# Performance work log

Hardware: AMD Instinct MI355X
Metric: run time of the kernel (lower is better)

Reference implementation:

```python
import jax, jax.numpy as jnp
import numpy as np

N_NODES = 100000
N_EDGES = 1600000
N_PAIRS = 200000
IN_C, HID_C, OUT_C = 128, 128, 64


def setup_inputs() -> dict:
    key = jax.random.key(0)
    ks = jax.random.split(key, 10)
    x = jax.random.normal(ks[0], (N_NODES, IN_C), dtype=jnp.float32)
    edge_index = jax.random.randint(ks[1], (2, N_EDGES), 0, N_NODES, dtype=jnp.int64)
    node_i = jax.random.randint(ks[2], (N_PAIRS,), 0, N_NODES, dtype=jnp.int64)
    node_j = jax.random.randint(ks[3], (N_PAIRS,), 0, N_NODES, dtype=jnp.int64)
    def glorot(k, fan_in, fan_out):
        s = jnp.sqrt(6.0 / (fan_in + fan_out))
        return jax.random.uniform(k, (fan_in, fan_out), jnp.float32, -s, s)
    W1 = glorot(ks[4], IN_C, HID_C)
    b1 = jnp.zeros((HID_C,), jnp.float32)
    W2 = glorot(ks[5], HID_C, HID_C)
    b2 = jnp.zeros((HID_C,), jnp.float32)
    W3 = glorot(ks[6], HID_C, OUT_C)
    b3 = jnp.zeros((OUT_C,), jnp.float32)
    return {"x": x, "edge_index": edge_index, "node_i": node_i, "node_j": node_j,
            "W1": W1, "b1": b1, "W2": W2, "b2": b2, "W3": W3, "b3": b3}


def _gcn_layer(h, src, dst, deg_inv, w_e, W, b):
    # h: [N, Cin] -> linear then symmetric-normalized aggregation (with self loops)
    h = h @ W  # [N, Cout]
    msg = h[src] * w_e[:, None]  # [E, Cout] gather + edge weight
    agg = jax.ops.segment_sum(msg, dst, num_segments=N_NODES)
    agg = agg + h * deg_inv[:, None]  # self-loop term: h_i / deg_i
    return agg + b


def reference(x, edge_index, node_i, node_j, W1, b1, W2, b2, W3, b3):
    src, dst = edge_index[0], edge_index[1]
    # GCN normalization with self loops: deg_i = 1 + in-degree
    ones = jnp.ones((N_EDGES,), jnp.float32)
    deg = jax.ops.segment_sum(ones, dst, num_segments=N_NODES) + 1.0
    dinv_sqrt = jax.lax.rsqrt(deg)
    deg_inv = 1.0 / deg
    w_e = dinv_sqrt[src] * dinv_sqrt[dst]  # [E]

    h = _gcn_layer(x, src, dst, deg_inv, w_e, W1, b1)
    h = jax.nn.relu(h)  # dropout is identity in eval mode
    h = _gcn_layer(h, src, dst, deg_inv, w_e, W2, b2)
    h = jax.nn.relu(h)
    h = _gcn_layer(h, src, dst, deg_inv, w_e, W3, b3)

    # dot-product link decode (decode_type=None)
    return jnp.sum(h[node_i] * h[node_j], axis=-1)  # [N_PAIRS]
```

## Files before the change

kernel.cpp:

```cpp
#include <hip/hip_runtime.h>

#define NN 100000
#define NNP 100032
#define NE 1600000
#define NP 200000
#define NBKT 782
#define BCAP 3072
#define BKB 4096

typedef short s16x8 __attribute__((ext_vector_type(8)));
typedef float f32x4 __attribute__((ext_vector_type(4)));
typedef float f32x2 __attribute__((ext_vector_type(2)));

__device__ __forceinline__ unsigned short f2bf(float f) {
  unsigned int u = __float_as_uint(f);
  u += 0x7fffu + ((u >> 16) & 1u);
  return (unsigned short)(u >> 16);
}

__device__ __forceinline__ void pkadd(f32x2& a, uint u) {
  f32x2 v;
  v.x = __uint_as_float(u << 16);
  v.y = __uint_as_float(u & 0xffff0000u);
  asm("v_pk_add_f32 %0, %0, %1" : "+v"(a) : "v"(v));
}

__device__ __forceinline__ void rowadd(uint4 v, f32x2* a) {
  pkadd(a[0], v.x);
  pkadd(a[1], v.y);
  pkadd(a[2], v.z);
  pkadd(a[3], v.w);
}

template <int RSH>
__device__ __forceinline__ void gath(const int* __restrict__ col,
                                     const char* __restrict__ Tb, int s,
                                     int tend, uint co, f32x2* acc) {
  const int d = tend - s;
  const int nfull = d >> 3;
  const int rem = d & 7;
  int e = s;
  int c[8];
#pragma unroll
  for (int j = 0; j < 8; ++j) c[j] = col[e + j];
#pragma unroll 1
  for (int it = 0; it < nfull; ++it) {
    uint4 v0 = *(const uint4*)(Tb + (((uint)c[0] << RSH) | co));
    uint4 v1 = *(const uint4*)(Tb + (((uint)c[1] << RSH) | co));
    uint4 v2 = *(const uint4*)(Tb + (((uint)c[2] << RSH) | co));
    uint4 v3 = *(const uint4*)(Tb + (((uint)c[3] << RSH) | co));
    uint4 v4 = *(const uint4*)(Tb + (((uint)c[4] << RSH) | co));
    uint4 v5 = *(const uint4*)(Tb + (((uint)c[5] << RSH) | co));
    uint4 v6 = *(const uint4*)(Tb + (((uint)c[6] << RSH) | co));
    uint4 v7 = *(const uint4*)(Tb + (((uint)c[7] << RSH) | co));
    e += 8;
#pragma unroll
    for (int j = 0; j < 8; ++j) c[j] = col[e + j];
    rowadd(v0, acc);
    rowadd(v1, acc);
    rowadd(v2, acc);
    rowadd(v3, acc);
    rowadd(v4, acc);
    rowadd(v5, acc);
    rowadd(v6, acc);
    rowadd(v7, acc);
  }
  if (rem) {
#pragma unroll
    for (int j = 0; j < 8; ++j) c[j] = (j < rem) ? c[j] : NN;
    uint4 v0 = *(const uint4*)(Tb + (((uint)c[0] << RSH) | co));
    uint4 v1 = *(const uint4*)(Tb + (((uint)c[1] << RSH) | co));
    uint4 v2 = *(const uint4*)(Tb + (((uint)c[2] << RSH) | co));
    uint4 v3 = *(const uint4*)(Tb + (((uint)c[3] << RSH) | co));
    uint4 v4 = *(const uint4*)(Tb + (((uint)c[4] << RSH) | co));
    uint4 v5 = *(const uint4*)(Tb + (((uint)c[5] << RSH) | co));
    uint4 v6 = *(const uint4*)(Tb + (((uint)c[6] << RSH) | co));
    uint4 v7 = *(const uint4*)(Tb + (((uint)c[7] << RSH) | co));
    rowadd(v0, acc);
    rowadd(v1, acc);
    rowadd(v2, acc);
    rowadd(v3, acc);
    rowadd(v4, acc);
    rowadd(v5, acc);
    rowadd(v6, acc);
    rowadd(v7, acc);
  }
}

template <int NT>
__device__ __forceinline__ void prepw_dev(const float* __restrict__ W,
                                          uint* __restrict__ Wt, int tid) {
  constexpr int COUT = NT * 16;
  if (tid >= 4 * NT * 64) return;
  int lane = tid & 63, comb = tid >> 6;
  int ks = comb / NT, tl = comb % NT;
  int q = lane >> 4, n = lane & 15;
  uint w[4];
#pragma unroll
  for (int jj = 0; jj < 4; ++jj) {
    int k0 = ks * 32 + q * 8 + 2 * jj;
    uint lo = f2bf(W[k0 * COUT + tl * 16 + n]);
    uint hi = f2bf(W[(k0 + 1) * COUT + tl * 16 + n]);
    w[jj] = lo | (hi << 16);
  }
  ((uint4*)Wt)[comb * 64 + lane] = make_uint4(w[0], w[1], w[2], w[3]);
}

__global__ __launch_bounds__(256) void k_setup(const float* __restrict__ W1,
                                               const float* __restrict__ W2,
                                               const float* __restrict__ W3,
                                               uint* __restrict__ Wt1,
                                               uint* __restrict__ Wt2,
                                               uint* __restrict__ Wt3,
                                               int* __restrict__ gcur) {
  int b = blockIdx.x, t = threadIdx.x;
  if (b < 4) {
    int i = b * 256 + t;
    if (i < 1024) gcur[i] = 0;
  } else if (b < 12) {
    prepw_dev<8>(W1, Wt1, (b - 4) * 256 + t);
  } else if (b < 20) {
    prepw_dev<8>(W2, Wt2, (b - 12) * 256 + t);
  } else {
    prepw_dev<4>(W3, Wt3, (b - 20) * 256 + t);
  }
}

__global__ __launch_bounds__(256) void k_bucket(const int* __restrict__ ei,
                                                int* __restrict__ gcur,
                                                int* __restrict__ aux) {
  __shared__ int cnt[1024];
  __shared__ int scn[1024];
  __shared__ int cur[1024];
  __shared__ int sc[256];
  __shared__ int sorted[BKB];
  __shared__ unsigned short sbkt[BKB];
  const int t = threadIdx.x;
  const int base = blockIdx.x * BKB;

  for (int i = t; i < 1024; i += 256) cnt[i] = 0;
  __syncthreads();

  int pk[16], bk[16];
#pragma unroll
  for (int i = 0; i < 16; ++i) {
    int e = base + t + 256 * i;
    if (e < NE) {
      int src = ei[e], dst = ei[NE + e];
      bk[i] = dst >> 7;
      pk[i] = src | ((dst & 127) << 17);
      atomicAdd(&cnt[bk[i]], 1);
    } else {
      bk[i] = -1;
    }
  }
  __syncthreads();

  int s0 = cnt[4 * t], s1 = cnt[4 * t + 1], s2 = cnt[4 * t + 2], s3 = cnt[4 * t + 3];
  int local = s0 + s1 + s2 + s3;
  sc[t] = local;
  __syncthreads();
  for (int off = 1; off < 256; off <<= 1) {
    int a = (t >= off) ? sc[t - off] : 0;
    __syncthreads();
    sc[t] += a;
    __syncthreads();
  }
  int b0 = sc[t] - local;
  scn[4 * t] = b0;
  scn[4 * t + 1] = b0 + s0;
  scn[4 * t + 2] = b0 + s0 + s1;
  scn[4 * t + 3] = b0 + s0 + s1 + s2;
  cur[4 * t] = scn[4 * t];
  cur[4 * t + 1] = scn[4 * t + 1];
  cur[4 * t + 2] = scn[4 * t + 2];
  cur[4 * t + 3] = scn[4 * t + 3];
  __syncthreads();
  const int tot = sc[255];

#pragma unroll
  for (int i = 0; i < 16; ++i) {
    if (bk[i] >= 0) {
      int pos = atomicAdd(&cur[bk[i]], 1);
      sorted[pos] = pk[i];
      sbkt[pos] = (unsigned short)bk[i];
    }
  }
  __syncthreads();

  for (int b = t; b < 1024; b += 256) {
    int c = cnt[b];
    if (c > 0) cur[b] = b * BCAP + atomicAdd(&gcur[b], c);
  }
  __syncthreads();

  for (int k = t; k < tot; k += 256) {
    int b = sbkt[k];
    aux[cur[b] + (k - scn[b])] = sorted[k];
  }
}

__global__ __launch_bounds__(256) void k_csr(const int* __restrict__ gcur,
                                             const int* __restrict__ aux,
                                             int* __restrict__ row_ptr,
                                             float* __restrict__ dinv,
                                             int* __restrict__ col) {
  __shared__ int red[256];
  __shared__ int c[128];
  __shared__ int cur[128];
  const int b = blockIdx.x, t = threadIdx.x;
  int p = 0;
  for (int i = t; i < b; i += 256) p += gcur[i];
  red[t] = p;
  if (t < 128) c[t] = 0;
  __syncthreads();
  for (int off = 128; off > 0; off >>= 1) {
    if (t < off) red[t] += red[t + off];
    __syncthreads();
  }
  const int base = red[0];
  const int m = gcur[b];
  const int* a = aux + (size_t)b * BCAP;
  __syncthreads();
  for (int k = t; k < m; k += 256) atomicAdd(&c[a[k] >> 17], 1);
  __syncthreads();
  int val = (t < 128) ? c[t] : 0;
  red[t] = val;
  __syncthreads();
  for (int off = 1; off < 128; off <<= 1) {
    int add = (t >= off && t < 128) ? red[t - off] : 0;
    __syncthreads();
    if (t < 128) red[t] += add;
    __syncthreads();
  }
  if (t < 128) {
    int excl = red[t] - val + base;
    int node = b * 128 + t;
    if (node < NN) {
      row_ptr[node] = excl;
      dinv[node] = rsqrtf((float)(val + 1));
      cur[t] = excl;
    }
  }
  if (b == NBKT - 1 && t == 0) row_ptr[NN] = base + m;
  __syncthreads();
  for (int k = t; k < m; k += 256) {
    int pk2 = a[k];
    int pos = atomicAdd(&cur[pk2 >> 17], 1);
    col[pos] = pk2 & 0x1FFFF;
  }
}

__global__ __launch_bounds__(256) void k_gemm1(const float* __restrict__ A,
                                               const uint* __restrict__ Wt,
                                               const float* __restrict__ dinv,
                                               unsigned short* __restrict__ T) {
  constexpr int NT = 8, COUT = 128;
  __shared__ __align__(16) uint Wlds[4 * NT * 64 * 4];
  __shared__ __align__(16) unsigned short Obuf[64 * COUT];
  const int t = threadIdx.x;
  {
    const uint4* src = (const uint4*)Wt;
    uint4* dst = (uint4*)Wlds;
    for (int i = t; i < 4 * NT * 64; i += 256) dst[i] = src[i];
  }
  __syncthreads();

  const int wv = t >> 6, lane = t & 63;
  const int n = lane & 15, quad = lane >> 4;
  const int rbase = blockIdx.x * 64 + wv * 16;

  union AB { uint4 u; s16x8 s; };
  AB a[4];
  {
    int row = rbase + n;
    if (row >= NN) row = NN - 1;
    const float* ap = A + (size_t)row * 128;
#pragma unroll
    for (int ks = 0; ks < 4; ++ks) {
      float4 v0 = *(const float4*)(ap + ks * 32 + quad * 8);
      float4 v1 = *(const float4*)(ap + ks * 32 + quad * 8 + 4);
      a[ks].u.x = (uint)f2bf(v0.x) | ((uint)f2bf(v0.y) << 16);
      a[ks].u.y = (uint)f2bf(v0.z) | ((uint)f2bf(v0.w) << 16);
      a[ks].u.z = (uint)f2bf(v1.x) | ((uint)f2bf(v1.y) << 16);
      a[ks].u.w = (uint)f2bf(v1.z) | ((uint)f2bf(v1.w) << 16);
    }
  }

  f32x4 acc[NT];
#pragma unroll
  for (int tl = 0; tl < NT; ++tl) acc[tl] = (f32x4){0.f, 0.f, 0.f, 0.f};

#pragma unroll
  for (int ks = 0; ks < 4; ++ks) {
#pragma unroll
    for (int tl = 0; tl < NT; ++tl) {
      AB b;
      b.u = *(const uint4*)&Wlds[((ks * NT + tl) * 64 + lane) * 4];
      acc[tl] = __builtin_amdgcn_mfma_f32_16x16x32_bf16(a[ks].s, b.s, acc[tl], 0, 0, 0);
    }
  }

  float4 dv = *(const float4*)(dinv + rbase + quad * 4);
  float dvv[4] = {dv.x, dv.y, dv.z, dv.w};
  unsigned short* ob = Obuf + wv * 16 * COUT;
#pragma unroll
  for (int tl = 0; tl < NT; ++tl)
#pragma unroll
    for (int r = 0; r < 4; ++r)
      ob[(quad * 4 + r) * COUT + tl * 16 + n] = f2bf(acc[tl][r] * dvv[r]);

  uint4* gdst = (uint4*)(T + (size_t)rbase * COUT);
#pragma unroll
  for (int i = 0; i < 4; ++i) {
    int off16 = i * 64 + lane;
    int lrow = (off16 * 8) / COUT;
    uint4 v = make_uint4(0u, 0u, 0u, 0u);
    if (rbase + lrow < NN) v = *(const uint4*)&ob[off16 * 8];
    gdst[off16] = v;
  }
}

template <int COUT>
__global__ __launch_bounds__(256) void k_gg(const int* __restrict__ row_ptr,
                                            const int* __restrict__ col,
                                            const uint4* __restrict__ T4,
                                            const float* __restrict__ dinv,
                                            const float* __restrict__ bias,
                                            const uint4* __restrict__ Wt,
                                            unsigned short* __restrict__ Tout) {
  constexpr int NT = COUT / 16;
  constexpr int TLW = NT / 4;
  constexpr int OSTR = COUT + 8;
  __shared__ __align__(16) uint4 Alds[16 * 17];
  const int t = threadIdx.x, wv = t >> 6, lane = t & 63;
  const int nbase = blockIdx.x * 16;
  const int q = lane >> 4, cl = lane & 15;

  const int node = nbase + wv * 4 + q;
  int s = 0, tend = 0;
  if (node < NN) {
    s = row_ptr[node];
    tend = row_ptr[node + 1];
  }
  const char* Tb = (const char*)T4;
  const uint co = (uint)cl << 4;
  f32x2 acc[4];
  acc[0] = (f32x2){0.f, 0.f};
  acc[1] = (f32x2){0.f, 0.f};
  acc[2] = (f32x2){0.f, 0.f};
  acc[3] = (f32x2){0.f, 0.f};
  rowadd(*(const uint4*)(Tb + (((uint)node << 8) | co)), acc);
  gath<8>(col, Tb, s, tend, co, acc);

  {
    float dv = dinv[node];
    float4 b0 = *(const float4*)&bias[cl * 8];
    float4 b1 = *(const float4*)&bias[cl * 8 + 4];
    float r0 = fmaxf(fmaf(dv, acc[0].x, b0.x), 0.f);
    float r1 = fmaxf(fmaf(dv, acc[0].y, b0.y), 0.f);
    float r2 = fmaxf(fmaf(dv, acc[1].x, b0.z), 0.f);
    float r3 = fmaxf(fmaf(dv, acc[1].y, b0.w), 0.f);
    float r4 = fmaxf(fmaf(dv, acc[2].x, b1.x), 0.f);
    float r5 = fmaxf(fmaf(dv, acc[2].y, b1.y), 0.f);
    float r6 = fmaxf(fmaf(dv, acc[3].x, b1.z), 0.f);
    float r7 = fmaxf(fmaf(dv, acc[3].y, b1.w), 0.f);
    uint4 o;
    o.x = (uint)f2bf(r0) | ((uint)f2bf(r1) << 16);
    o.y = (uint)f2bf(r2) | ((uint)f2bf(r3) << 16);
    o.z = (uint)f2bf(r4) | ((uint)f2bf(r5) << 16);
    o.w = (uint)f2bf(r6) | ((uint)f2bf(r7) << 16);
    Alds[(wv * 4 + q) * 17 + cl] = o;
  }
  __syncthreads();

  const int n = lane & 15, quad = lane >> 4;
  union AB { uint4 u; s16x8 s; };
  AB a[4];
#pragma unroll
  for (int ks = 0; ks < 4; ++ks) a[ks].u = Alds[n * 17 + ks * 4 + quad];
  f32x4 acc2[TLW];
#pragma unroll
  for (int j = 0; j < TLW; ++j) acc2[j] = (f32x4){0.f, 0.f, 0.f, 0.f};
#pragma unroll
  for (int ks = 0; ks < 4; ++ks) {
#pragma unroll
    for (int j = 0; j < TLW; ++j) {
      int tl = wv * TLW + j;
      AB b;
      b.u = Wt[(ks * NT + tl) * 64 + lane];
      acc2[j] = __builtin_amdgcn_mfma_f32_16x16x32_bf16(a[ks].s, b.s, acc2[j], 0, 0, 0);
    }
  }
  __syncthreads();

  unsigned short* Obuf = (unsigned short*)Alds;
  float4 dv4 = *(const float4*)(dinv + nbase + quad * 4);
  float dvv[4] = {dv4.x, dv4.y, dv4.z, dv4.w};
#pragma unroll
  for (int j = 0; j < TLW; ++j) {
    int tl = wv * TLW + j;
#pragma unroll
    for (int r = 0; r < 4; ++r)
      Obuf[(quad * 4 + r) * OSTR + tl * 16 + n] = f2bf(acc2[j][r] * dvv[r]);
  }
  __syncthreads();

  if constexpr (COUT == 128) {
    int row = t >> 4, c16 = t & 15;
    uint4 v = make_uint4(0u, 0u, 0u, 0u);
    if (nbase + row < NN) v = *(const uint4*)&Obuf[row * OSTR + c16 * 8];
    ((uint4*)(Tout + (size_t)nbase * COUT))[row * 16 + c16] = v;
  } else {
    if (t < 128) {
      int row = t >> 3, c16 = t & 7;
      uint4 v = make_uint4(0u, 0u, 0u, 0u);
      if (nbase + row < NN) v = *(const uint4*)&Obuf[row * OSTR + c16 * 8];
      ((uint4*)(Tout + (size_t)nbase * COUT))[row * 8 + c16] = v;
    }
  }
}

__global__ __launch_bounds__(256) void k_gather3(const int* __restrict__ row_ptr,
                                                 const int* __restrict__ col,
                                                 const uint4* __restrict__ T4,
                                                 uint4* __restrict__ G3) {
  const int wid = (blockIdx.x * 256 + threadIdx.x) >> 6;
  const int lane = threadIdx.x & 63;
  const int g = lane >> 3, cl = lane & 7;
  const int node = wid * 8 + g;
  if (node >= NN) return;
  int s = row_ptr[node], tend = row_ptr[node + 1];
  const char* Tb = (const char*)T4;
  const uint co = (uint)cl << 4;
  f32x2 acc[4];
  acc[0] = (f32x2){0.f, 0.f};
  acc[1] = (f32x2){0.f, 0.f};
  acc[2] = (f32x2){0.f, 0.f};
  acc[3] = (f32x2){0.f, 0.f};
  rowadd(*(const uint4*)(Tb + (((uint)node << 7) | co)), acc);
  gath<7>(col, Tb, s, tend, co, acc);
  uint4 o;
  o.x = (uint)f2bf(acc[0].x) | ((uint)f2bf(acc[0].y) << 16);
  o.y = (uint)f2bf(acc[1].x) | ((uint)f2bf(acc[1].y) << 16);
  o.z = (uint)f2bf(acc[2].x) | ((uint)f2bf(acc[2].y) << 16);
  o.w = (uint)f2bf(acc[3].x) | ((uint)f2bf(acc[3].y) << 16);
  G3[(size_t)node * 8 + cl] = o;
}

__global__ __launch_bounds__(256) void k_decode(const int* __restrict__ ni,
                                                const int* __restrict__ nj,
                                                const uint2* __restrict__ G3,
                                                const float* __restrict__ dinv,
                                                const float* __restrict__ b3,
                                                float* __restrict__ out) {
  int p = blockIdx.x * 16 + (threadIdx.x >> 4);
  int cl = threadIdx.x & 15;
  int i = ni[p], j = nj[p];
  uint2 ui = G3[(size_t)i * 16 + cl];
  uint2 uj = G3[(size_t)j * 16 + cl];
  float4 bb = *(const float4*)&b3[cl * 4];
  float di = dinv[i], dj = dinv[j];
  float gi0 = __uint_as_float(ui.x << 16), gi1 = __uint_as_float(ui.x & 0xffff0000u);
  float gi2 = __uint_as_float(ui.y << 16), gi3 = __uint_as_float(ui.y & 0xffff0000u);
  float gj0 = __uint_as_float(uj.x << 16), gj1 = __uint_as_float(uj.x & 0xffff0000u);
  float gj2 = __uint_as_float(uj.y << 16), gj3 = __uint_as_float(uj.y & 0xffff0000u);
  float v = fmaf(di, gi0, bb.x) * fmaf(dj, gj0, bb.x) +
            fmaf(di, gi1, bb.y) * fmaf(dj, gj1, bb.y) +
            fmaf(di, gi2, bb.z) * fmaf(dj, gj2, bb.z) +
            fmaf(di, gi3, bb.w) * fmaf(dj, gj3, bb.w);
  v += __shfl_xor(v, 1, 64);
  v += __shfl_xor(v, 2, 64);
  v += __shfl_xor(v, 4, 64);
  v += __shfl_xor(v, 8, 64);
  if (cl == 0) out[p] = v;
}

extern "C" void kernel_launch(void* const* d_in, const int* in_sizes, int n_in,
                              void* d_out, int out_size, void* d_ws, size_t ws_size,
                              hipStream_t stream) {
  const float* x  = (const float*)d_in[0];
  const int*   ei = (const int*)d_in[1];
  const int*   ni = (const int*)d_in[2];
  const int*   nj = (const int*)d_in[3];
  const float* W1 = (const float*)d_in[4];
  const float* b1 = (const float*)d_in[5];
  const float* W2 = (const float*)d_in[6];
  const float* b2 = (const float*)d_in[7];
  const float* W3 = (const float*)d_in[8];
  const float* b3 = (const float*)d_in[9];
  float* out = (float*)d_out;

  float* dinv    = (float*)d_ws;
  int*   row_ptr = (int*)(dinv + 102400);
  int*   gcur    = row_ptr + 102400;
  int*   col     = gcur + 1024;
  uint*  Wt1     = (uint*)(col + NE);
  uint*  Wt2     = Wt1 + 8192;
  uint*  Wt3     = Wt2 + 8192;
  uint*  Tbf     = Wt3 + 4096;
  uint*  T2      = Tbf + (size_t)NNP * 64;
  uint*  G3      = T2 + (size_t)NNP * 64;
  int*   aux     = (int*)G3;

  k_setup<<<24, 256, 0, stream>>>(W1, W2, W3, Wt1, Wt2, Wt3, gcur);
  k_bucket<<<(NE + BKB - 1) / BKB, 256, 0, stream>>>(ei, gcur, aux);
  k_csr<<<NBKT, 256, 0, stream>>>(gcur, aux, row_ptr, dinv, col);

  const int GB = NNP / 64;
  const int FB = NNP / 16;
  const int GATB = NN / 32;

  k_gemm1<<<GB, 256, 0, stream>>>(x, Wt1, dinv, (unsigned short*)Tbf);
  k_gg<128><<<FB, 256, 0, stream>>>(row_ptr, col, (const uint4*)Tbf, dinv, b1,
                                    (const uint4*)Wt2, (unsigned short*)T2);
  k_gg<64><<<FB, 256, 0, stream>>>(row_ptr, col, (const uint4*)T2, dinv, b2,
                                   (const uint4*)Wt3, (unsigned short*)Tbf);
  k_gather3<<<GATB, 256, 0, stream>>>(row_ptr, col, (const uint4*)Tbf, (uint4*)G3);
  k_decode<<<NP / 16, 256, 0, stream>>>(ni, nj, (const uint2*)G3, dinv, b3, out);
}
```

Baseline: 305.5 us.

## Process nodes in degree-sorted order in aggregation kernels for load balance

Builds a degree histogram during CSR construction, scans it, and computes a permutation that groups nodes by in-degree. The fused gather+GEMM kernels and the final gather kernel then process nodes in this permuted order, so wavefronts handle neighbors of similar length and lanes within a wave diverge less. Output rows are scattered back to original node positions. This adds two small kernels, extra indirection loads, and loses contiguous output stores and locality of self-row reads.

```diff
diff --git a/kernel.cpp b/kernel.cpp
--- a/kernel.cpp
+++ b/kernel.cpp
@@ -112,7 +112,8 @@
                                                uint* __restrict__ Wt1,
                                                uint* __restrict__ Wt2,
                                                uint* __restrict__ Wt3,
-                                               int* __restrict__ gcur) {
+                                               int* __restrict__ gcur,
+                                               int* __restrict__ dhist) {
   int b = blockIdx.x, t = threadIdx.x;
   if (b < 4) {
     int i = b * 256 + t;
@@ -121,8 +122,10 @@
     prepw_dev<8>(W1, Wt1, (b - 4) * 256 + t);
   } else if (b < 20) {
     prepw_dev<8>(W2, Wt2, (b - 12) * 256 + t);
+  } else if (b < 24) {
+    prepw_dev<4>(W3, Wt3, (b - 20) * 256 + t);
   } else {
-    prepw_dev<4>(W3, Wt3, (b - 20) * 256 + t);
+    for (int i = t; i < 2048; i += 256) dhist[i] = 0;
   }
 }
 
@@ -204,11 +207,14 @@
                                              const int* __restrict__ aux,
                                              int* __restrict__ row_ptr,
                                              float* __restrict__ dinv,
-                                             int* __restrict__ col) {
+                                             int* __restrict__ col,
+                                             int* __restrict__ dhist) {
   __shared__ int red[256];
   __shared__ int c[128];
   __shared__ int cur[128];
+  __shared__ int lh[1024];
   const int b = blockIdx.x, t = threadIdx.x;
+  for (int i = t; i < 1024; i += 256) lh[i] = 0;
   int p = 0;
   for (int i = t; i < b; i += 256) p += gcur[i];
   red[t] = p;
@@ -240,6 +246,7 @@
       row_ptr[node] = excl;
       dinv[node] = rsqrtf((float)(val + 1));
       cur[t] = excl;
+      atomicAdd(&lh[min(val, 1023)], 1);
     }
   }
   if (b == NBKT - 1 && t == 0) row_ptr[NN] = base + m;
@@ -249,6 +256,60 @@
     int pos = atomicAdd(&cur[pk2 >> 17], 1);
     col[pos] = pk2 & 0x1FFFF;
   }
+  for (int i = t; i < 1024; i += 256)
+    if (lh[i]) atomicAdd(&dhist[i], lh[i]);
+}
+
+__global__ __launch_bounds__(256) void k_scan(const int* __restrict__ dhist,
+                                              int* __restrict__ dbase,
+                                              int* __restrict__ perm) {
+  __shared__ int sc[256];
+  const int t = threadIdx.x;
+  int v0 = dhist[4 * t], v1 = dhist[4 * t + 1];
+  int v2 = dhist[4 * t + 2], v3 = dhist[4 * t + 3];
+  int loc = v0 + v1 + v2 + v3;
+  sc[t] = loc;
+  __syncthreads();
+  for (int off = 1; off < 256; off <<= 1) {
+    int a = (t >= off) ? sc[t - off] : 0;
+    __syncthreads();
+    sc[t] += a;
+    __syncthreads();
+  }
+  int b0 = sc[t] - loc;
+  dbase[4 * t] = b0;
+  dbase[4 * t + 1] = b0 + v0;
+  dbase[4 * t + 2] = b0 + v0 + v1;
+  dbase[4 * t + 3] = b0 + v0 + v1 + v2;
+  if (t < NNP - NN) perm[NN + t] = NN;
+}
+
+__global__ __launch_bounds__(256) void k_perm(const int* __restrict__ row_ptr,
+                                              int* __restrict__ dbase,
+                                              int* __restrict__ perm) {
+  __shared__ int lh[1024];
+  __shared__ int lb[1024];
+  const int t = threadIdx.x;
+  const int nb = blockIdx.x * 1024;
+  for (int i = t; i < 1024; i += 256) lh[i] = 0;
+  __syncthreads();
+  int dg[4], rk[4];
+#pragma unroll
+  for (int i = 0; i < 4; ++i) {
+    int node = nb + i * 256 + t;
+    dg[i] = -1;
+    if (node < NN) {
+      int d = row_ptr[node + 1] - row_ptr[node];
+      dg[i] = min(d, 1023);
+      rk[i] = atomicAdd(&lh[dg[i]], 1);
+    }
+  }
+  __syncthreads();
+  for (int i = t; i < 1024; i += 256) lb[i] = lh[i] ? atomicAdd(&dbase[i], lh[i]) : 0;
+  __syncthreads();
+#pragma unroll
+  for (int i = 0; i < 4; ++i)
+    if (dg[i] >= 0) perm[lb[dg[i]] + rk[i]] = nb + i * 256 + t;
 }
 
 __global__ __launch_bounds__(256) void k_gemm1(const float* __restrict__ A,
@@ -328,6 +389,7 @@
                                             const float* __restrict__ dinv,
                                             const float* __restrict__ bias,
                                             const uint4* __restrict__ Wt,
+                                            const int* __restrict__ perm,
                                             unsigned short* __restrict__ Tout) {
   constexpr int NT = COUT / 16;
   constexpr int TLW = NT / 4;
@@ -337,7 +399,7 @@
   const int nbase = blockIdx.x * 16;
   const int q = lane >> 4, cl = lane & 15;
 
-  const int node = nbase + wv * 4 + q;
+  const int node = perm[nbase + wv * 4 + q];
   int s = 0, tend = 0;
   if (node < NN) {
     s = row_ptr[node];
@@ -395,8 +457,9 @@
   __syncthreads();
 
   unsigned short* Obuf = (unsigned short*)Alds;
-  float4 dv4 = *(const float4*)(dinv + nbase + quad * 4);
-  float dvv[4] = {dv4.x, dv4.y, dv4.z, dv4.w};
+  float dvv[4];
+#pragma unroll
+  for (int r = 0; r < 4; ++r) dvv[r] = dinv[perm[nbase + quad * 4 + r]];
 #pragma unroll
   for (int j = 0; j < TLW; ++j) {
     int tl = wv * TLW + j;
@@ -408,15 +471,17 @@
 
   if constexpr (COUT == 128) {
     int row = t >> 4, c16 = t & 15;
+    int nr = perm[nbase + row];
     uint4 v = make_uint4(0u, 0u, 0u, 0u);
     if (nbase + row < NN) v = *(const uint4*)&Obuf[row * OSTR + c16 * 8];
-    ((uint4*)(Tout + (size_t)nbase * COUT))[row * 16 + c16] = v;
+    ((uint4*)(Tout + (size_t)nr * COUT))[c16] = v;
   } else {
     if (t < 128) {
       int row = t >> 3, c16 = t & 7;
+      int nr = perm[nbase + row];
       uint4 v = make_uint4(0u, 0u, 0u, 0u);
       if (nbase + row < NN) v = *(const uint4*)&Obuf[row * OSTR + c16 * 8];
-      ((uint4*)(Tout + (size_t)nbase * COUT))[row * 8 + c16] = v;
+      ((uint4*)(Tout + (size_t)nr * COUT))[c16] = v;
     }
   }
 }
@@ -424,12 +489,14 @@
 __global__ __launch_bounds__(256) void k_gather3(const int* __restrict__ row_ptr,
                                                  const int* __restrict__ col,
                                                  const uint4* __restrict__ T4,
+                                                 const int* __restrict__ perm,
                                                  uint4* __restrict__ G3) {
   const int wid = (blockIdx.x * 256 + threadIdx.x) >> 6;
   const int lane = threadIdx.x & 63;
   const int g = lane >> 3, cl = lane & 7;
-  const int node = wid * 8 + g;
-  if (node >= NN) return;
+  const int slot = wid * 8 + g;
+  if (slot >= NN) return;
+  const int node = perm[slot];
   int s = row_ptr[node], tend = row_ptr[node + 1];
   const char* Tb = (const char*)T4;
   const uint co = (uint)cl << 4;
@@ -501,11 +568,16 @@
   uint*  Tbf     = Wt3 + 4096;
   uint*  T2      = Tbf + (size_t)NNP * 64;
   uint*  G3      = T2 + (size_t)NNP * 64;
+  int*   perm    = (int*)(G3 + (size_t)NNP * 32);
+  int*   dhist   = perm + NNP;
+  int*   dbase   = dhist + 1024;
   int*   aux     = (int*)G3;
 
-  k_setup<<<24, 256, 0, stream>>>(W1, W2, W3, Wt1, Wt2, Wt3, gcur);
+  k_setup<<<25, 256, 0, stream>>>(W1, W2, W3, Wt1, Wt2, Wt3, gcur, dhist);
   k_bucket<<<(NE + BKB - 1) / BKB, 256, 0, stream>>>(ei, gcur, aux);
-  k_csr<<<NBKT, 256, 0, stream>>>(gcur, aux, row_ptr, dinv, col);
+  k_csr<<<NBKT, 256, 0, stream>>>(gcur, aux, row_ptr, dinv, col, dhist);
+  k_scan<<<1, 256, 0, stream>>>(dhist, dbase, perm);
+  k_perm<<<(NN + 1023) / 1024, 256, 0, stream>>>(row_ptr, dbase, perm);
 
   const int GB = NNP / 64;
   const int FB = NNP / 16;
@@ -513,9 +585,9 @@
 
   k_gemm1<<<GB, 256, 0, stream>>>(x, Wt1, dinv, (unsigned short*)Tbf);
   k_gg<128><<<FB, 256, 0, stream>>>(row_ptr, col, (const uint4*)Tbf, dinv, b1,
-                                    (const uint4*)Wt2, (unsigned short*)T2);
+                                    (const uint4*)Wt2, perm, (unsigned short*)T2);
   k_gg<64><<<FB, 256, 0, stream>>>(row_ptr, col, (const uint4*)T2, dinv, b2,
-                                   (const uint4*)Wt3, (unsigned short*)Tbf);
-  k_gather3<<<GATB, 256, 0, stream>>>(row_ptr, col, (const uint4*)Tbf, (uint4*)G3);
+                                   (const uint4*)Wt3, perm, (unsigned short*)Tbf);
+  k_gather3<<<GATB, 256, 0, stream>>>(row_ptr, col, (const uint4*)Tbf, perm, (uint4*)G3);
   k_decode<<<NP / 16, 256, 0, stream>>>(ni, nj, (const uint2*)G3, dinv, b3, out);
 }
```

Measured after the change: 326.6 us. +6.9%, slower.

## Shard feature tables by channel slice so each gather pass hits a cache-resident slice

Applied to the files above, without the earlier changes.

The feature tables move from row-major to a channel-sliced layout (8 slices of 32 bytes per node, or 16 bytes for the last layer). Aggregation kernels now process one slice per block group, so the gathered working set per pass is much smaller and more likely to stay in L2/MALL. The fused gather+GEMM kernel is split into separate transform (MFMA) and aggregate kernels. Column-index loads and output stores are marked nontemporal. In exchange the adjacency is read eight times and there are more kernel launches, and each gather now moves only 16–32 bytes per access, which may use memory less efficiently.

```diff
diff --git a/kernel.cpp b/kernel.cpp
--- a/kernel.cpp
+++ b/kernel.cpp
@@ -11,6 +11,7 @@
 typedef short s16x8 __attribute__((ext_vector_type(8)));
 typedef float f32x4 __attribute__((ext_vector_type(4)));
 typedef float f32x2 __attribute__((ext_vector_type(2)));
+typedef uint u32x4 __attribute__((ext_vector_type(4)));
 
 __device__ __forceinline__ unsigned short f2bf(float f) {
   unsigned int u = __float_as_uint(f);
@@ -30,6 +31,12 @@
   pkadd(a[1], v.y);
   pkadd(a[2], v.z);
   pkadd(a[3], v.w);
+}
+
+__device__ __forceinline__ void ntstore16(void* p, uint4 o) {
+  u32x4 v;
+  v.x = o.x; v.y = o.y; v.z = o.z; v.w = o.w;
+  __builtin_nontemporal_store(v, (u32x4*)p);
 }
 
 template <int RSH>
@@ -42,7 +49,7 @@
   int e = s;
   int c[8];
 #pragma unroll
-  for (int j = 0; j < 8; ++j) c[j] = col[e + j];
+  for (int j = 0; j < 8; ++j) c[j] = __builtin_nontemporal_load(&col[e + j]);
 #pragma unroll 1
   for (int it = 0; it < nfull; ++it) {
     uint4 v0 = *(const uint4*)(Tb + (((uint)c[0] << RSH) | co));
@@ -55,7 +62,7 @@
     uint4 v7 = *(const uint4*)(Tb + (((uint)c[7] << RSH) | co));
     e += 8;
 #pragma unroll
-    for (int j = 0; j < 8; ++j) c[j] = col[e + j];
+    for (int j = 0; j < 8; ++j) c[j] = __builtin_nontemporal_load(&col[e + j]);
     rowadd(v0, acc);
     rowadd(v1, acc);
     rowadd(v2, acc);
@@ -251,52 +258,53 @@
   }
 }
 
-__global__ __launch_bounds__(256) void k_gemm1(const float* __restrict__ A,
-                                               const uint* __restrict__ Wt,
+template <int COUT, bool INF32>
+__global__ __launch_bounds__(256) void k_trans(const char* __restrict__ Ain,
+                                               const uint4* __restrict__ Wt,
                                                const float* __restrict__ dinv,
-                                               unsigned short* __restrict__ T) {
-  constexpr int NT = 8, COUT = 128;
-  __shared__ __align__(16) uint Wlds[4 * NT * 64 * 4];
+                                               uint4* __restrict__ Tsh) {
+  constexpr int NT = COUT / 16;
   __shared__ __align__(16) unsigned short Obuf[64 * COUT];
-  const int t = threadIdx.x;
-  {
-    const uint4* src = (const uint4*)Wt;
-    uint4* dst = (uint4*)Wlds;
-    for (int i = t; i < 4 * NT * 64; i += 256) dst[i] = src[i];
-  }
-  __syncthreads();
-
-  const int wv = t >> 6, lane = t & 63;
+  const int t = threadIdx.x, wv = t >> 6, lane = t & 63;
   const int n = lane & 15, quad = lane >> 4;
-  const int rbase = blockIdx.x * 64 + wv * 16;
+  const int brow = blockIdx.x * 64;
+  const int rbase = brow + wv * 16;
 
   union AB { uint4 u; s16x8 s; };
   AB a[4];
   {
     int row = rbase + n;
     if (row >= NN) row = NN - 1;
-    const float* ap = A + (size_t)row * 128;
-#pragma unroll
-    for (int ks = 0; ks < 4; ++ks) {
-      float4 v0 = *(const float4*)(ap + ks * 32 + quad * 8);
-      float4 v1 = *(const float4*)(ap + ks * 32 + quad * 8 + 4);
-      a[ks].u.x = (uint)f2bf(v0.x) | ((uint)f2bf(v0.y) << 16);
-      a[ks].u.y = (uint)f2bf(v0.z) | ((uint)f2bf(v0.w) << 16);
-      a[ks].u.z = (uint)f2bf(v1.x) | ((uint)f2bf(v1.y) << 16);
-      a[ks].u.w = (uint)f2bf(v1.z) | ((uint)f2bf(v1.w) << 16);
+    if constexpr (INF32) {
+      const float* ap = (const float*)Ain + (size_t)row * 128;
+#pragma unroll
+      for (int ks = 0; ks < 4; ++ks) {
+        float4 v0 = *(const float4*)(ap + ks * 32 + quad * 8);
+        float4 v1 = *(const float4*)(ap + ks * 32 + quad * 8 + 4);
+        a[ks].u.x = (uint)f2bf(v0.x) | ((uint)f2bf(v0.y) << 16);
+        a[ks].u.y = (uint)f2bf(v0.z) | ((uint)f2bf(v0.w) << 16);
+        a[ks].u.z = (uint)f2bf(v1.x) | ((uint)f2bf(v1.y) << 16);
+        a[ks].u.w = (uint)f2bf(v1.z) | ((uint)f2bf(v1.w) << 16);
+      }
+    } else {
+#pragma unroll
+      for (int ks = 0; ks < 4; ++ks) {
+        int ch = ks * 4 + quad;
+        a[ks].u = *(const uint4*)(Ain + (size_t)(ch >> 1) * (NNP * 32) +
+                                  (uint)row * 32 + (ch & 1) * 16);
+      }
     }
   }
 
   f32x4 acc[NT];
 #pragma unroll
   for (int tl = 0; tl < NT; ++tl) acc[tl] = (f32x4){0.f, 0.f, 0.f, 0.f};
-
 #pragma unroll
   for (int ks = 0; ks < 4; ++ks) {
 #pragma unroll
     for (int tl = 0; tl < NT; ++tl) {
       AB b;
-      b.u = *(const uint4*)&Wlds[((ks * NT + tl) * 64 + lane) * 4];
+      b.u = Wt[(ks * NT + tl) * 64 + lane];
       acc[tl] = __builtin_amdgcn_mfma_f32_16x16x32_bf16(a[ks].s, b.s, acc[tl], 0, 0, 0);
     }
   }
@@ -309,143 +317,92 @@
 #pragma unroll
     for (int r = 0; r < 4; ++r)
       ob[(quad * 4 + r) * COUT + tl * 16 + n] = f2bf(acc[tl][r] * dvv[r]);
-
-  uint4* gdst = (uint4*)(T + (size_t)rbase * COUT);
-#pragma unroll
-  for (int i = 0; i < 4; ++i) {
-    int off16 = i * 64 + lane;
-    int lrow = (off16 * 8) / COUT;
-    uint4 v = make_uint4(0u, 0u, 0u, 0u);
-    if (rbase + lrow < NN) v = *(const uint4*)&ob[off16 * 8];
-    gdst[off16] = v;
-  }
-}
-
-template <int COUT>
-__global__ __launch_bounds__(256) void k_gg(const int* __restrict__ row_ptr,
-                                            const int* __restrict__ col,
-                                            const uint4* __restrict__ T4,
-                                            const float* __restrict__ dinv,
-                                            const float* __restrict__ bias,
-                                            const uint4* __restrict__ Wt,
-                                            unsigned short* __restrict__ Tout) {
-  constexpr int NT = COUT / 16;
-  constexpr int TLW = NT / 4;
-  constexpr int OSTR = COUT + 8;
-  __shared__ __align__(16) uint4 Alds[16 * 17];
-  const int t = threadIdx.x, wv = t >> 6, lane = t & 63;
-  const int nbase = blockIdx.x * 16;
-  const int q = lane >> 4, cl = lane & 15;
-
-  const int node = nbase + wv * 4 + q;
-  int s = 0, tend = 0;
-  if (node < NN) {
-    s = row_ptr[node];
-    tend = row_ptr[node + 1];
-  }
-  const char* Tb = (const char*)T4;
-  const uint co = (uint)cl << 4;
+  __syncthreads();
+
+  const int s = t >> 5, id32 = t & 31;
+  if constexpr (COUT == 128) {
+#pragma unroll
+    for (int it = 0; it < 4; ++it) {
+      int idx = it * 32 + id32;
+      int r = idx >> 1, h = idx & 1;
+      uint4 v = make_uint4(0u, 0u, 0u, 0u);
+      if (brow + r < NN) v = *(const uint4*)&Obuf[r * COUT + s * 16 + h * 8];
+      Tsh[(size_t)s * (NNP * 2) + (brow + r) * 2 + h] = v;
+    }
+  } else {
+#pragma unroll
+    for (int it = 0; it < 2; ++it) {
+      int r = it * 32 + id32;
+      uint4 v = make_uint4(0u, 0u, 0u, 0u);
+      if (brow + r < NN) v = *(const uint4*)&Obuf[r * COUT + s * 8];
+      Tsh[(size_t)s * NNP + brow + r] = v;
+    }
+  }
+}
+
+__global__ __launch_bounds__(256) void k_agg(const int* __restrict__ row_ptr,
+                                             const int* __restrict__ col,
+                                             const char* __restrict__ Tsh,
+                                             const float* __restrict__ dinv,
+                                             const float* __restrict__ bias,
+                                             uint4* __restrict__ Hsh) {
+  const int t = threadIdx.x;
+  const int s = blockIdx.x & 7, tile = blockIdx.x >> 3;
+  const int node = tile * 128 + (t >> 1);
+  const int h = t & 1;
+  if (node >= NN) return;
+  const char* Tb = Tsh + (size_t)s * (NNP * 32);
+  const uint co = (uint)h << 4;
   f32x2 acc[4];
   acc[0] = (f32x2){0.f, 0.f};
   acc[1] = (f32x2){0.f, 0.f};
   acc[2] = (f32x2){0.f, 0.f};
   acc[3] = (f32x2){0.f, 0.f};
-  rowadd(*(const uint4*)(Tb + (((uint)node << 8) | co)), acc);
-  gath<8>(col, Tb, s, tend, co, acc);
-
-  {
-    float dv = dinv[node];
-    float4 b0 = *(const float4*)&bias[cl * 8];
-    float4 b1 = *(const float4*)&bias[cl * 8 + 4];
-    float r0 = fmaxf(fmaf(dv, acc[0].x, b0.x), 0.f);
-    float r1 = fmaxf(fmaf(dv, acc[0].y, b0.y), 0.f);
-    float r2 = fmaxf(fmaf(dv, acc[1].x, b0.z), 0.f);
-    float r3 = fmaxf(fmaf(dv, acc[1].y, b0.w), 0.f);
-    float r4 = fmaxf(fmaf(dv, acc[2].x, b1.x), 0.f);
-    float r5 = fmaxf(fmaf(dv, acc[2].y, b1.y), 0.f);
-    float r6 = fmaxf(fmaf(dv, acc[3].x, b1.z), 0.f);
-    float r7 = fmaxf(fmaf(dv, acc[3].y, b1.w), 0.f);
-    uint4 o;
-    o.x = (uint)f2bf(r0) | ((uint)f2bf(r1) << 16);
-    o.y = (uint)f2bf(r2) | ((uint)f2bf(r3) << 16);
-    o.z = (uint)f2bf(r4) | ((uint)f2bf(r5) << 16);
-    o.w = (uint)f2bf(r6) | ((uint)f2bf(r7) << 16);
-    Alds[(wv * 4 + q) * 17 + cl] = o;
-  }
-  __syncthreads();
-
-  const int n = lane & 15, quad = lane >> 4;
-  union AB { uint4 u; s16x8 s; };
-  AB a[4];
-#pragma unroll
-  for (int ks = 0; ks < 4; ++ks) a[ks].u = Alds[n * 17 + ks * 4 + quad];
-  f32x4 acc2[TLW];
-#pragma unroll
-  for (int j = 0; j < TLW; ++j) acc2[j] = (f32x4){0.f, 0.f, 0.f, 0.f};
-#pragma unroll
-  for (int ks = 0; ks < 4; ++ks) {
-#pragma unroll
-    for (int j = 0; j < TLW; ++j) {
-      int tl = wv * TLW + j;
-      AB b;
-      b.u = Wt[(ks * NT + tl) * 64 + lane];
-      acc2[j] = __builtin_amdgcn_mfma_f32_16x16x32_bf16(a[ks].s, b.s, acc2[j], 0, 0, 0);
-    }
-  }
-  __syncthreads();
-
-  unsigned short* Obuf = (unsigned short*)Alds;
-  float4 dv4 = *(const float4*)(dinv + nbase + quad * 4);
-  float dvv[4] = {dv4.x, dv4.y, dv4.z, dv4.w};
-#pragma unroll
-  for (int j = 0; j < TLW; ++j) {
-    int tl = wv * TLW + j;
-#pragma unroll
-    for (int r = 0; r < 4; ++r)
-      Obuf[(quad * 4 + r) * OSTR + tl * 16 + n] = f2bf(acc2[j][r] * dvv[r]);
-  }
-  __syncthreads();
-
-  if constexpr (COUT == 128) {
-    int row = t >> 4, c16 = t & 15;
-    uint4 v = make_uint4(0u, 0u, 0u, 0u);
-    if (nbase + row < NN) v = *(const uint4*)&Obuf[row * OSTR + c16 * 8];
-    ((uint4*)(Tout + (size_t)nbase * COUT))[row * 16 + c16] = v;
-  } else {
-    if (t < 128) {
-      int row = t >> 3, c16 = t & 7;
-      uint4 v = make_uint4(0u, 0u, 0u, 0u);
-      if (nbase + row < NN) v = *(const uint4*)&Obuf[row * OSTR + c16 * 8];
-      ((uint4*)(Tout + (size_t)nbase * COUT))[row * 8 + c16] = v;
-    }
-  }
-}
-
-__global__ __launch_bounds__(256) void k_gather3(const int* __restrict__ row_ptr,
-                                                 const int* __restrict__ col,
-                                                 const uint4* __restrict__ T4,
-                                                 uint4* __restrict__ G3) {
-  const int wid = (blockIdx.x * 256 + threadIdx.x) >> 6;
-  const int lane = threadIdx.x & 63;
-  const int g = lane >> 3, cl = lane & 7;
-  const int node = wid * 8 + g;
+  rowadd(*(const uint4*)(Tb + (((uint)node << 5) | co)), acc);
+  gath<5>(col, Tb, row_ptr[node], row_ptr[node + 1], co, acc);
+
+  float dvx = dinv[node];
+  const float* bp = bias + s * 16 + h * 8;
+  float4 b0 = *(const float4*)bp;
+  float4 b1 = *(const float4*)(bp + 4);
+  float r0 = fmaxf(fmaf(dvx, acc[0].x, b0.x), 0.f);
+  float r1 = fmaxf(fmaf(dvx, acc[0].y, b0.y), 0.f);
+  float r2 = fmaxf(fmaf(dvx, acc[1].x, b0.z), 0.f);
+  float r3 = fmaxf(fmaf(dvx, acc[1].y, b0.w), 0.f);
+  float r4 = fmaxf(fmaf(dvx, acc[2].x, b1.x), 0.f);
+  float r5 = fmaxf(fmaf(dvx, acc[2].y, b1.y), 0.f);
+  float r6 = fmaxf(fmaf(dvx, acc[3].x, b1.z), 0.f);
+  float r7 = fmaxf(fmaf(dvx, acc[3].y, b1.w), 0.f);
+  uint4 o;
+  o.x = (uint)f2bf(r0) | ((uint)f2bf(r1) << 16);
+  o.y = (uint)f2bf(r2) | ((uint)f2bf(r3) << 16);
+  o.z = (uint)f2bf(r4) | ((uint)f2bf(r5) << 16);
+  o.w = (uint)f2bf(r6) | ((uint)f2bf(r7) << 16);
+  ntstore16(&Hsh[(size_t)s * (NNP * 2) + node * 2 + h], o);
+}
+
+__global__ __launch_bounds__(256) void k_agg3(const int* __restrict__ row_ptr,
+                                              const int* __restrict__ col,
+                                              const char* __restrict__ Tsh,
+                                              char* __restrict__ G3) {
+  const int t = threadIdx.x;
+  const int s = blockIdx.x & 7, tile = blockIdx.x >> 3;
+  const int node = tile * 256 + t;
   if (node >= NN) return;
-  int s = row_ptr[node], tend = row_ptr[node + 1];
-  const char* Tb = (const char*)T4;
-  const uint co = (uint)cl << 4;
+  const char* Tb = Tsh + (size_t)s * (NNP * 16);
   f32x2 acc[4];
   acc[0] = (f32x2){0.f, 0.f};
   acc[1] = (f32x2){0.f, 0.f};
   acc[2] = (f32x2){0.f, 0.f};
   acc[3] = (f32x2){0.f, 0.f};
-  rowadd(*(const uint4*)(Tb + (((uint)node << 7) | co)), acc);
-  gath<7>(col, Tb, s, tend, co, acc);
+  rowadd(*(const uint4*)(Tb + ((uint)node << 4)), acc);
+  gath<4>(col, Tb, row_ptr[node], row_ptr[node + 1], 0u, acc);
   uint4 o;
   o.x = (uint)f2bf(acc[0].x) | ((uint)f2bf(acc[0].y) << 16);
   o.y = (uint)f2bf(acc[1].x) | ((uint)f2bf(acc[1].y) << 16);
   o.z = (uint)f2bf(acc[2].x) | ((uint)f2bf(acc[2].y) << 16);
   o.w = (uint)f2bf(acc[3].x) | ((uint)f2bf(acc[3].y) << 16);
-  G3[(size_t)node * 8 + cl] = o;
+  ntstore16(G3 + (size_t)node * 128 + s * 16, o);
 }
 
 __global__ __launch_bounds__(256) void k_decode(const int* __restrict__ ni,
@@ -498,24 +455,24 @@
   uint*  Wt1     = (uint*)(col + NE);
   uint*  Wt2     = Wt1 + 8192;
   uint*  Wt3     = Wt2 + 8192;
-  uint*  Tbf     = Wt3 + 4096;
-  uint*  T2      = Tbf + (size_t)NNP * 64;
-  uint*  G3      = T2 + (size_t)NNP * 64;
+  uint*  Tsh     = Wt3 + 4096;
+  uint*  Hsh     = Tsh + (size_t)NNP * 64;
+  uint*  G3      = Hsh + (size_t)NNP * 64;
   int*   aux     = (int*)G3;
 
   k_setup<<<24, 256, 0, stream>>>(W1, W2, W3, Wt1, Wt2, Wt3, gcur);
   k_bucket<<<(NE + BKB - 1) / BKB, 256, 0, stream>>>(ei, gcur, aux);
   k_csr<<<NBKT, 256, 0, stream>>>(gcur, aux, row_ptr, dinv, col);
 
-  const int GB = NNP / 64;
-  const int FB = NNP / 16;
-  const int GATB = NN / 32;
-
-  k_gemm1<<<GB, 256, 0, stream>>>(x, Wt1, dinv, (unsigned short*)Tbf);
-  k_gg<128><<<FB, 256, 0, stream>>>(row_ptr, col, (const uint4*)Tbf, dinv, b1,
-                                    (const uint4*)Wt2, (unsigned short*)T2);
-  k_gg<64><<<FB, 256, 0, stream>>>(row_ptr, col, (const uint4*)T2, dinv, b2,
-                                   (const uint4*)Wt3, (unsigned short*)Tbf);
-  k_gather3<<<GATB, 256, 0, stream>>>(row_ptr, col, (const uint4*)Tbf, (uint4*)G3);
+  const int TB = NNP / 64;
+  const int AB_ = ((NN + 127) / 128) * 8;
+  const int A3B = ((NN + 255) / 256) * 8;
+
+  k_trans<128, true><<<TB, 256, 0, stream>>>((const char*)x, (const uint4*)Wt1, dinv, (uint4*)Tsh);
+  k_agg<<<AB_, 256, 0, stream>>>(row_ptr, col, (const char*)Tsh, dinv, b1, (uint4*)Hsh);
+  k_trans<128, false><<<TB, 256, 0, stream>>>((const char*)Hsh, (const uint4*)Wt2, dinv, (uint4*)Tsh);
+  k_agg<<<AB_, 256, 0, stream>>>(row_ptr, col, (const char*)Tsh, dinv, b2, (uint4*)Hsh);
+  k_trans<64, false><<<TB, 256, 0, stream>>>((const char*)Hsh, (const uint4*)Wt3, dinv, (uint4*)Tsh);
+  k_agg3<<<A3B, 256, 0, stream>>>(row_ptr, col, (const char*)Tsh, (char*)G3);
   k_decode<<<NP / 16, 256, 0, stream>>>(ni, nj, (const uint2*)G3, dinv, b3, out);
 }
```

New measurement: 496.2 us. 62.4% more time.
